# Performance work log

Hardware: AMD Instinct MI355X
Metric: run time of the kernel (lower is better)

## Reference

```python
import jax, jax.numpy as jnp
import numpy as np

S, B, V, E, H, C = 512, 64, 50000, 300, 256, 5


def setup_inputs() -> dict:
    key = jax.random.key(0)
    ks = jax.random.split(key, 8)
    return {
        "inputs": jax.random.randint(ks[0], (S, B), 0, V, dtype=jnp.int64),
        "emb": jax.random.normal(ks[1], (V, E), dtype=jnp.float32),
        # small weight scale to keep tanh out of saturation (matches typical init scale)
        "W_ih": jax.random.normal(ks[2], (H, E), dtype=jnp.float32) * 0.05,
        "W_hh": jax.random.normal(ks[3], (H, H), dtype=jnp.float32) * 0.05,
        "b_ih": jax.random.normal(ks[4], (H,), dtype=jnp.float32) * 0.05,
        "b_hh": jax.random.normal(ks[5], (H,), dtype=jnp.float32) * 0.05,
        "W_out": jax.random.normal(ks[6], (C, H), dtype=jnp.float32) * 0.05,
        "b_out": jax.random.normal(ks[7], (C,), dtype=jnp.float32) * 0.05,
    }


def reference(inputs, emb, W_ih, W_hh, b_ih, b_hh, W_out, b_out):
    # embedding lookup: (S, B, E)
    x = emb[inputs]
    # precompute input-to-hidden projection for all timesteps: (S, B, H)
    xW = jnp.einsum("sbe,he->sbh", x, W_ih) + b_ih

    def step(h, xw_t):
        h_new = jnp.tanh(xw_t + h @ W_hh.T + b_hh)
        return h_new, h_new

    h0 = jnp.zeros((inputs.shape[1], W_hh.shape[0]), dtype=x.dtype)
    _, rnn_out = jax.lax.scan(step, h0, xW)  # (S, B, H)

    logits = jnp.einsum("sbh,ch->sbc", rnn_out, W_out) + b_out  # (S, B, C)
    summed = logits.sum(axis=0)  # (B, C)
    return jax.nn.log_softmax(summed, axis=1)
```

## Files before the change

### kernel.cpp

```cpp
#include <hip/hip_runtime.h>
#include <stdint.h>

#define S_ 512
#define B_ 64
#define V_ 50000
#define E_ 300
#define H_ 256
#define C_ 5

typedef _Float16 h8_t __attribute__((ext_vector_type(8)));
typedef float f32x4 __attribute__((ext_vector_type(4)));

__device__ __forceinline__ float fast_tanh(float x) {
    float e = __builtin_amdgcn_exp2f(x * 2.88539008177793f);
    return fmaf(-2.0f, __builtin_amdgcn_rcpf(e + 1.0f), 1.0f);
}

__device__ __forceinline__ h8_t load_wfrag(const float* __restrict__ W,
                                           int h, int e0) {
    h8_t v;
    if (e0 + 8 <= E_) {
        float4 f0 = *(const float4*)(W + (size_t)h * E_ + e0);
        float4 f1 = *(const float4*)(W + (size_t)h * E_ + e0 + 4);
        v[0] = (_Float16)f0.x; v[1] = (_Float16)f0.y;
        v[2] = (_Float16)f0.z; v[3] = (_Float16)f0.w;
        v[4] = (_Float16)f1.x; v[5] = (_Float16)f1.y;
        v[6] = (_Float16)f1.z; v[7] = (_Float16)f1.w;
    } else if (e0 < E_) {
        float4 f0 = *(const float4*)(W + (size_t)h * E_ + e0);
        v[0] = (_Float16)f0.x; v[1] = (_Float16)f0.y;
        v[2] = (_Float16)f0.z; v[3] = (_Float16)f0.w;
        v[4] = (_Float16)0.0f; v[5] = (_Float16)0.0f;
        v[6] = (_Float16)0.0f; v[7] = (_Float16)0.0f;
    } else {
        v = (h8_t)(_Float16)0.0f;
    }
    return v;
}

__global__ __launch_bounds__(512, 2) void xw_kernel(
    const int* __restrict__ idx, const float* __restrict__ emb,
    const float* __restrict__ W_ih, const float* __restrict__ b_ih,
    const float* __restrict__ b_hh, float* __restrict__ xw) {
    __shared__ uint4 Afrag[4 * 10 * 64];
    const int tid = threadIdx.x;
    const int w = tid >> 6;
    const int l = tid & 63;
    const int n = l & 15;
    const int hi = l >> 4;
    const int base = blockIdx.x * 64;

    h8_t bw0[10], bw1[10];
#pragma unroll
    for (int ks = 0; ks < 10; ++ks) {
        bw0[ks] = load_wfrag(W_ih, (2 * w) * 16 + n, ks * 32 + hi * 8);
        bw1[ks] = load_wfrag(W_ih, (2 * w + 1) * 16 + n, ks * 32 + hi * 8);
    }
    const float bias0 = b_ih[w * 32 + n] + b_hh[w * 32 + n];
    const float bias1 = b_ih[w * 32 + 16 + n] + b_hh[w * 32 + 16 + n];

    for (int cc = tid; cc < 64 * 40; cc += 512) {
        int m = cc / 40;
        int c = cc - m * 40;
        int ks = c >> 2;
        int hic = c & 3;
        const float* src = emb + (size_t)idx[base + m] * E_ + 8 * c;
        h8_t v;
        if (c < 37) {
            float4 f0 = *(const float4*)src;
            float4 f1 = *(const float4*)(src + 4);
            v[0] = (_Float16)f0.x; v[1] = (_Float16)f0.y;
            v[2] = (_Float16)f0.z; v[3] = (_Float16)f0.w;
            v[4] = (_Float16)f1.x; v[5] = (_Float16)f1.y;
            v[6] = (_Float16)f1.z; v[7] = (_Float16)f1.w;
        } else if (c == 37) {
            float4 f0 = *(const float4*)src;
            v[0] = (_Float16)f0.x; v[1] = (_Float16)f0.y;
            v[2] = (_Float16)f0.z; v[3] = (_Float16)f0.w;
            v[4] = (_Float16)0.0f; v[5] = (_Float16)0.0f;
            v[6] = (_Float16)0.0f; v[7] = (_Float16)0.0f;
        } else {
            v = (h8_t)(_Float16)0.0f;
        }
        int fl = (hic << 4) | (m & 15);
        int mt = m >> 4;
        Afrag[(mt * 10 + ks) * 64 + fl] = __builtin_bit_cast(uint4, v);
    }
    __syncthreads();

    f32x4 c[4][2];
#pragma unroll
    for (int mt = 0; mt < 4; ++mt) {
        c[mt][0] = (f32x4)bias0;
        c[mt][1] = (f32x4)bias1;
    }
#pragma unroll
    for (int ks = 0; ks < 10; ++ks) {
#pragma unroll
        for (int mt = 0; mt < 4; ++mt) {
            h8_t a = __builtin_bit_cast(h8_t, Afrag[(mt * 10 + ks) * 64 + l]);
            c[mt][0] = __builtin_amdgcn_mfma_f32_16x16x32_f16(a, bw0[ks],
                                                              c[mt][0], 0, 0, 0);
            c[mt][1] = __builtin_amdgcn_mfma_f32_16x16x32_f16(a, bw1[ks],
                                                              c[mt][1], 0, 0, 0);
        }
    }
#pragma unroll
    for (int mt = 0; mt < 4; ++mt)
#pragma unroll
        for (int q = 0; q < 2; ++q) {
            float* op =
                xw + (size_t)(base + mt * 16 + hi * 4) * H_ + w * 32 + q * 16 + n;
#pragma unroll
            for (int r = 0; r < 4; ++r) op[(size_t)r * H_] = c[mt][q][r];
        }
}

__global__ __launch_bounds__(512, 2) void rnn_kernel(
    const float* __restrict__ xw, const float* __restrict__ W_hh,
    const float* __restrict__ W_out, const float* __restrict__ b_out,
    float* __restrict__ out) {
    const int tid = threadIdx.x;
    const int w = tid >> 6;
    const int l = tid & 63;
    const int n = l & 15;
    const int hi = l >> 4;
    const int col = n & 7;
    const int sel = n >> 3;
    const int bbase = blockIdx.x * 8;
    const int rowbase = w * 32;

    __shared__ __attribute__((aligned(16))) unsigned char smem[8192];
    char* lds = (char*)smem;

    h8_t a[2][8];
#pragma unroll
    for (int mt = 0; mt < 2; ++mt) {
        const float* wr = W_hh + (size_t)(rowbase + mt * 16 + n) * H_;
#pragma unroll
        for (int ks = 0; ks < 8; ++ks) {
            const float* wp = wr + ks * 32 + hi * 8;
            float4 f0 = *(const float4*)wp;
            float4 f1 = *(const float4*)(wp + 4);
            h8_t v;
            v[0] = (_Float16)f0.x; v[1] = (_Float16)f0.y;
            v[2] = (_Float16)f0.z; v[3] = (_Float16)f0.w;
            v[4] = (_Float16)f1.x; v[5] = (_Float16)f1.y;
            v[6] = (_Float16)f1.z; v[7] = (_Float16)f1.w;
            a[mt][ks] = v;
        }
    }

    const int wboff =
        (w * 4 + sel * 2 + (hi >> 1)) * 128 + col * 16 + (hi & 1) * 8;
    const int rdbase = hi * 128 + col * 16;

    for (int t = tid; t < 1024; t += 512) ((unsigned int*)lds)[t] = 0u;

    f32x4 hs = (f32x4)0.0f;

    const float* xwl = xw + (size_t)(bbase + col) * H_ + rowbase + hi * 4;
    f32x4 cv[4][2];
    cv[0][0] = *(const f32x4*)(xwl);
    cv[0][1] = *(const f32x4*)(xwl + 16);
    cv[1][0] = *(const f32x4*)(xwl + 16384);
    cv[1][1] = *(const f32x4*)(xwl + 16384 + 16);
    __syncthreads();

#define STEP(CUR, I, SBASE)                                                    \
    {                                                                          \
        int sp = (SBASE) + 2;                                                  \
        if (sp > S_ - 1) sp = S_ - 1;                                          \
        cv[(I + 2) & 3][0] = *(const f32x4*)(xwl + (size_t)sp * 16384);        \
        cv[(I + 2) & 3][1] = *(const f32x4*)(xwl + (size_t)sp * 16384 + 16);   \
        h8_t bf[8];                                                            \
        _Pragma("unroll") for (int ks = 0; ks < 8; ++ks)                       \
            bf[ks] = *(const h8_t*)(lds + (CUR)*4096 + rdbase + ks * 512);     \
        _Pragma("unroll") for (int ks = 0; ks < 8; ++ks) {                     \
            cv[I][0] = __builtin_amdgcn_mfma_f32_16x16x32_f16(                 \
                a[0][ks], bf[ks], cv[I][0], 0, 0, 0);                          \
            cv[I][1] = __builtin_amdgcn_mfma_f32_16x16x32_f16(                 \
                a[1][ks], bf[ks], cv[I][1], 0, 0, 0);                          \
        }                                                                      \
        {                                                                      \
            f32x4 sv = (sel == 0) ? cv[I][0] : cv[I][1];                       \
            float h0 = fast_tanh(sv[0]);                                       \
            float h1 = fast_tanh(sv[1]);                                       \
            float h2 = fast_tanh(sv[2]);                                       \
            float h3 = fast_tanh(sv[3]);                                       \
            hs[0] += h0; hs[1] += h1; hs[2] += h2; hs[3] += h3;                \
            uint2 pk;                                                          \
            pk.x = __builtin_bit_cast(unsigned int,                            \
                                      __builtin_amdgcn_cvt_pkrtz(h0, h1));     \
            pk.y = __builtin_bit_cast(unsigned int,                            \
                                      __builtin_amdgcn_cvt_pkrtz(h2, h3));     \
            *(uint2*)(lds + ((CUR) ^ 1) * 4096 + wboff) = pk;                  \
        }                                                                      \
        asm volatile("s_waitcnt lgkmcnt(0)" ::: "memory");                     \
        __builtin_amdgcn_s_barrier();                                          \
    }

    for (int s = 0; s < S_; s += 4) {
        STEP(0, 0, s)
        STEP(1, 1, s + 1)
        STEP(0, 2, s + 2)
        STEP(1, 3, s + 3)
    }
#undef STEP

    {
        const int k0v = rowbase + sel * 16 + hi * 4;
        *(f32x4*)(lds + col * 1024 + k0v * 4) = hs;
    }
    __syncthreads();
    {
        const float* hrow = (const float*)(lds + w * 1024);
        float lg[C_];
#pragma unroll
        for (int c = 0; c < C_; ++c) {
            float p = 0.0f;
#pragma unroll
            for (int q = 0; q < 4; ++q)
                p = fmaf(hrow[l + 64 * q], W_out[c * H_ + l + 64 * q], p);
#pragma unroll
            for (int off = 32; off; off >>= 1) p += __shfl_xor(p, off);
            lg[c] = p + (float)S_ * b_out[c];
        }
        if (l == 0) {
            float m = lg[0];
#pragma unroll
            for (int c = 1; c < C_; ++c) m = fmaxf(m, lg[c]);
            float sum = 0.0f;
#pragma unroll
            for (int c = 0; c < C_; ++c) sum += expf(lg[c] - m);
            float lse = logf(sum);
#pragma unroll
            for (int c = 0; c < C_; ++c)
                out[(bbase + w) * C_ + c] = lg[c] - m - lse;
        }
    }
}

extern "C" void kernel_launch(void* const* d_in, const int* in_sizes, int n_in,
                              void* d_out, int out_size, void* d_ws,
                              size_t ws_size, hipStream_t stream) {
    const int* idx = (const int*)d_in[0];
    const float* emb = (const float*)d_in[1];
    const float* W_ih = (const float*)d_in[2];
    const float* W_hh = (const float*)d_in[3];
    const float* b_ih = (const float*)d_in[4];
    const float* b_hh = (const float*)d_in[5];
    const float* W_out = (const float*)d_in[6];
    const float* b_out = (const float*)d_in[7];
    float* out = (float*)d_out;

    float* xw = (float*)d_ws;

    hipLaunchKernelGGL(xw_kernel, dim3((S_ * B_) / 64), dim3(512), 0, stream,
                       idx, emb, W_ih, b_ih, b_hh, xw);
    hipLaunchKernelGGL(rnn_kernel, dim3(8), dim3(512), 0, stream, xw, W_hh,
                       W_out, b_out, out);
}
```

Measured before the change: 266.0 us.

## Split recurrent kernel across 16 blocks of 1024 threads, 4 batch columns each

Reworks the sequential RNN recurrence so each block handles 4 batch columns instead of 8, with 16 waves each owning 16 hidden rows and one MFMA chain per step. This halves the per-wave MFMA chain length on the latency-bound serial timestep path and spreads work over twice as many CUs. In exchange, each wave applies tanh to one selected element per lane, barriers span 16 waves, and half the MFMA output columns go unused, so the MFMA work is less efficient.

Measured after the change: 265.7 us. No clear change (-0.1%).

```diff
diff --git a/kernel.cpp b/kernel.cpp
--- a/kernel.cpp
+++ b/kernel.cpp
@@ -116,7 +116,7 @@
         }
 }
 
-__global__ __launch_bounds__(512, 2) void rnn_kernel(
+__global__ __launch_bounds__(1024, 4) void rnn_kernel(
     const float* __restrict__ xw, const float* __restrict__ W_hh,
     const float* __restrict__ W_out, const float* __restrict__ b_out,
     float* __restrict__ out) {
@@ -125,18 +125,16 @@
     const int l = tid & 63;
     const int n = l & 15;
     const int hi = l >> 4;
-    const int col = n & 7;
-    const int sel = n >> 3;
-    const int bbase = blockIdx.x * 8;
-    const int rowbase = w * 32;
-
-    __shared__ __attribute__((aligned(16))) unsigned char smem[8192];
+    const int col = n & 3;
+    const int d = n >> 2;
+    const int bbase = blockIdx.x * 4;
+
+    __shared__ __attribute__((aligned(16))) unsigned char smem[4096];
     char* lds = (char*)smem;
 
-    h8_t a[2][8];
-#pragma unroll
-    for (int mt = 0; mt < 2; ++mt) {
-        const float* wr = W_hh + (size_t)(rowbase + mt * 16 + n) * H_;
+    h8_t a[8];
+    {
+        const float* wr = W_hh + (size_t)(w * 16 + n) * H_;
 #pragma unroll
         for (int ks = 0; ks < 8; ++ks) {
             const float* wp = wr + ks * 32 + hi * 8;
@@ -147,54 +145,46 @@
             v[2] = (_Float16)f0.z; v[3] = (_Float16)f0.w;
             v[4] = (_Float16)f1.x; v[5] = (_Float16)f1.y;
             v[6] = (_Float16)f1.z; v[7] = (_Float16)f1.w;
-            a[mt][ks] = v;
-        }
-    }
-
+            a[ks] = v;
+        }
+    }
+
+    const int k0 = w * 16 + hi * 4 + d;
     const int wboff =
-        (w * 4 + sel * 2 + (hi >> 1)) * 128 + col * 16 + (hi & 1) * 8;
-    const int rdbase = hi * 128 + col * 16;
-
-    for (int t = tid; t < 1024; t += 512) ((unsigned int*)lds)[t] = 0u;
-
-    f32x4 hs = (f32x4)0.0f;
-
-    const float* xwl = xw + (size_t)(bbase + col) * H_ + rowbase + hi * 4;
-    f32x4 cv[4][2];
-    cv[0][0] = *(const f32x4*)(xwl);
-    cv[0][1] = *(const f32x4*)(xwl + 16);
-    cv[1][0] = *(const f32x4*)(xwl + 16384);
-    cv[1][1] = *(const f32x4*)(xwl + 16384 + 16);
+        (k0 >> 5) * 256 + ((k0 >> 3) & 3) * 64 + col * 16 + (k0 & 7) * 2;
+    const int rdbase = hi * 64 + col * 16;
+
+    if (tid < 512) ((unsigned int*)lds)[tid] = 0u;
+
+    float hs = 0.0f;
+
+    const float* xwl = xw + (size_t)(bbase + col) * H_ + w * 16 + hi * 4;
+    f32x4 cv[4];
+    cv[0] = *(const f32x4*)(xwl);
+    cv[1] = *(const f32x4*)(xwl + 16384);
     __syncthreads();
 
 #define STEP(CUR, I, SBASE)                                                    \
     {                                                                          \
         int sp = (SBASE) + 2;                                                  \
         if (sp > S_ - 1) sp = S_ - 1;                                          \
-        cv[(I + 2) & 3][0] = *(const f32x4*)(xwl + (size_t)sp * 16384);        \
-        cv[(I + 2) & 3][1] = *(const f32x4*)(xwl + (size_t)sp * 16384 + 16);   \
+        cv[(I + 2) & 3] = *(const f32x4*)(xwl + (size_t)sp * 16384);           \
         h8_t bf[8];                                                            \
         _Pragma("unroll") for (int ks = 0; ks < 8; ++ks)                       \
-            bf[ks] = *(const h8_t*)(lds + (CUR)*4096 + rdbase + ks * 512);     \
+            bf[ks] = *(const h8_t*)(lds + (CUR)*2048 + rdbase + ks * 256);     \
         _Pragma("unroll") for (int ks = 0; ks < 8; ++ks) {                     \
-            cv[I][0] = __builtin_amdgcn_mfma_f32_16x16x32_f16(                 \
-                a[0][ks], bf[ks], cv[I][0], 0, 0, 0);                          \
-            cv[I][1] = __builtin_amdgcn_mfma_f32_16x16x32_f16(                 \
-                a[1][ks], bf[ks], cv[I][1], 0, 0, 0);                          \
+            cv[I] = __builtin_amdgcn_mfma_f32_16x16x32_f16(a[ks], bf[ks],      \
+                                                           cv[I], 0, 0, 0);    \
         }                                                                      \
         {                                                                      \
-            f32x4 sv = (sel == 0) ? cv[I][0] : cv[I][1];                       \
-            float h0 = fast_tanh(sv[0]);                                       \
-            float h1 = fast_tanh(sv[1]);                                       \
-            float h2 = fast_tanh(sv[2]);                                       \
-            float h3 = fast_tanh(sv[3]);                                       \
-            hs[0] += h0; hs[1] += h1; hs[2] += h2; hs[3] += h3;                \
-            uint2 pk;                                                          \
-            pk.x = __builtin_bit_cast(unsigned int,                            \
-                                      __builtin_amdgcn_cvt_pkrtz(h0, h1));     \
-            pk.y = __builtin_bit_cast(unsigned int,                            \
-                                      __builtin_amdgcn_cvt_pkrtz(h2, h3));     \
-            *(uint2*)(lds + ((CUR) ^ 1) * 4096 + wboff) = pk;                  \
+            f32x4 sv = cv[I];                                                  \
+            float e0 = (d == 1) ? sv[1] : sv[0];                               \
+            e0 = (d == 2) ? sv[2] : e0;                                        \
+            e0 = (d == 3) ? sv[3] : e0;                                        \
+            float h0 = fast_tanh(e0);                                          \
+            hs += h0;                                                          \
+            *(unsigned short*)(lds + ((CUR) ^ 1) * 2048 + wboff) =             \
+                __builtin_bit_cast(unsigned short, (_Float16)h0);              \
         }                                                                      \
         asm volatile("s_waitcnt lgkmcnt(0)" ::: "memory");                     \
         __builtin_amdgcn_s_barrier();                                          \
@@ -208,12 +198,10 @@
     }
 #undef STEP
 
-    {
-        const int k0v = rowbase + sel * 16 + hi * 4;
-        *(f32x4*)(lds + col * 1024 + k0v * 4) = hs;
-    }
-    __syncthreads();
-    {
+    __syncthreads();
+    *(float*)(lds + col * 1024 + k0 * 4) = hs;
+    __syncthreads();
+    if (w < 4) {
         const float* hrow = (const float*)(lds + w * 1024);
         float lg[C_];
 #pragma unroll
@@ -258,6 +246,6 @@
 
     hipLaunchKernelGGL(xw_kernel, dim3((S_ * B_) / 64), dim3(512), 0, stream,
                        idx, emb, W_ih, b_ih, b_hh, xw);
-    hipLaunchKernelGGL(rnn_kernel, dim3(8), dim3(512), 0, stream, xw, W_hh,
+    hipLaunchKernelGGL(rnn_kernel, dim3(16), dim3(1024), 0, stream, xw, W_hh,
                        W_out, b_out, out);
 }
```
